# Performance work log

Hardware: AMD Instinct MI355X
Metric: run time of the kernel (lower is better)

## Reference

```python
import jax, jax.numpy as jnp
import numpy as np

SPARSITY = 0.8
LOCAL_WINDOW = 64


def setup_inputs() -> dict:
    key = jax.random.key(0)
    k1, k2 = jax.random.split(key)
    B, H, S = 2, 8, 2048
    attention_scores = jax.random.normal(k1, (B, H, S, S), dtype=jnp.float32)
    rand_u = jax.random.uniform(k2, (B, H, S, S), dtype=jnp.float32)
    return {"attention_scores": attention_scores, "rand_u": rand_u}


def reference(attention_scores, rand_u):
    B, H, S, _ = attention_scores.shape
    dt = attention_scores.dtype
    half = LOCAL_WINDOW // 2
    k = max(1, int(S * (1.0 - SPARSITY)))

    idx = jnp.arange(S)
    # local window mask: row i covers columns [max(0,i-half), min(S,i+half))
    local = ((idx[None, :] >= idx[:, None] - half) & (idx[None, :] < idx[:, None] + half)).astype(dt)  # (S,S)

    # global mask: topk over head-averaged importance, shared across heads
    importance = attention_scores.mean(axis=1)  # (B,S,S)
    _, top_g = jax.lax.top_k(importance, k)  # (B,S,k)
    gmask = jnp.zeros((B, S, S), dtype=dt).at[
        jnp.arange(B)[:, None, None], jnp.arange(S)[None, :, None], top_g
    ].set(1.0)

    # random sparsification mask
    random_mask = (rand_u < (1.0 - SPARSITY)).astype(dt)

    combined = ((local[None, None, :, :] + gmask[:, None, :, :] + random_mask) > 0).astype(dt)

    # sparsity enforcement: per-row topk of masked scores -> binary mask
    masked = attention_scores * combined
    _, top_f = jax.lax.top_k(masked, k)  # (B,H,S,k)
    final = jnp.zeros((B, H, S, S), dtype=dt).at[
        jnp.arange(B)[:, None, None, None],
        jnp.arange(H)[None, :, None, None],
        jnp.arange(S)[None, None, :, None],
        top_f,
    ].set(1.0)
    return final
```

## Files before the change

kernel.cpp:

```cpp
#include <hip/hip_runtime.h>
#include <cstdint>
#include <cstddef>

#define S_LEN   2048
#define N_HEADS 8
#define N_BATCH 2
#define TOPK    409
#define HALF_WIN 32
#define KEY_P0  0x80000000u
#define KEY_N0  0x7FFFFFFFu

__device__ __forceinline__ unsigned mbcnt64(unsigned long long m) {
  return __builtin_amdgcn_mbcnt_hi((unsigned)(m >> 32),
         __builtin_amdgcn_mbcnt_lo((unsigned)m, 0u));
}

__device__ __forceinline__ void radix_range(const unsigned (&keys)[32], unsigned kk0,
                                            bool pos, unsigned* h, int l,
                                            unsigned& T_ret, unsigned& kk_ret,
                                            bool& cnt1) {
  unsigned prefix = 0, done = 0, kk = kk0;
  unsigned T = 0;
  bool resolved = false;
  cnt1 = false;
  #pragma unroll
  for (int pass = 0; pass < 4; ++pass) {
    const int shift = 24 - 8 * pass;
    *(uint4*)&h[l * 4] = make_uint4(0, 0, 0, 0);
    __threadfence_block();
    #pragma unroll
    for (int q = 0; q < 32; ++q) {
      unsigned kj = keys[q];
      bool in = pos ? (kj > KEY_P0) : (kj < KEY_N0);
      if (in && (kj & done) == prefix)
        atomicAdd(&h[(kj >> shift) & 255u], 1u);
    }
    __threadfence_block();
    uint4 hv = *(const uint4*)&h[l * 4];
    unsigned s3 = hv.w;
    unsigned s2 = hv.z + s3;
    unsigned s1 = hv.y + s2;
    unsigned s0 = hv.x + s1;
    unsigned inc = s0;
    #pragma unroll
    for (int d = 1; d < 64; d <<= 1) {
      unsigned o = __shfl_down(inc, d);
      inc += (l + d < 64) ? o : 0u;
    }
    const unsigned tail = inc - s0;
    const unsigned ge[4] = {s0 + tail, s1 + tail, s2 + tail, s3 + tail};
    const unsigned gt[4] = {s1 + tail, s2 + tail, s3 + tail, tail};
    unsigned packed = 0;
    bool found = false;
    #pragma unroll
    for (int q = 0; q < 4; ++q) {
      if (gt[q] < kk && kk <= ge[q]) {
        packed = ((unsigned)(4 * l + q) << 24) | ((ge[q] - gt[q]) << 12) | (kk - gt[q]);
        found = true;
      }
    }
    unsigned long long bal = __ballot(found);
    int srcl = __ffsll((long long)bal) - 1;
    packed = __shfl(packed, srcl);
    const unsigned cnt = (packed >> 12) & 0xFFFu;
    kk = packed & 0xFFFu;
    prefix |= (packed >> 24) << shift;
    done |= 0xFFu << shift;
    if (cnt == 1u) {
      unsigned cand = 0;
      #pragma unroll
      for (int q = 0; q < 32; ++q) {
        unsigned kj = keys[q];
        bool in = pos ? (kj > KEY_P0) : (kj < KEY_N0);
        if (in && (kj & done) == prefix) cand = kj;
      }
      #pragma unroll
      for (int d = 1; d < 64; d <<= 1) cand |= __shfl_xor(cand, d);
      T = cand;
      resolved = true;
      cnt1 = true;
      break;
    }
  }
  if (!resolved) T = prefix;
  T_ret = T;
  kk_ret = kk;
}

__device__ __forceinline__ void resolve_T(const unsigned (&keys)[32], unsigned* h,
                                          int l, unsigned& T, unsigned& kk,
                                          bool& cnt1) {
  unsigned np = 0;
  #pragma unroll
  for (int q = 0; q < 32; ++q)
    np += (unsigned)__popcll(__ballot(keys[q] > KEY_P0));
  if (TOPK <= np) {
    radix_range(keys, TOPK, true, h, l, T, kk, cnt1);
  } else {
    unsigned n0 = 0, n1 = 0;
    #pragma unroll
    for (int q = 0; q < 32; ++q) {
      n0 += (unsigned)__popcll(__ballot(keys[q] == KEY_P0));
      n1 += (unsigned)__popcll(__ballot(keys[q] == KEY_N0));
    }
    if (TOPK <= np + n0)           { T = KEY_P0; kk = TOPK - np;      cnt1 = (n0 == 1); }
    else if (TOPK <= np + n0 + n1) { T = KEY_N0; kk = TOPK - np - n0; cnt1 = (n1 == 1); }
    else radix_range(keys, TOPK - np - n0 - n1, false, h, l, T, kk, cnt1);
  }
}

__device__ __forceinline__ unsigned select_bits(const unsigned (&keys)[32],
                                                unsigned T, unsigned kk,
                                                bool cnt1, int l) {
  unsigned bits = 0;
  if (cnt1) {
    #pragma unroll
    for (int q = 0; q < 32; ++q)
      bits |= (keys[q] >= T ? 1u : 0u) << q;
    return bits;
  }
  unsigned S_tot = 0;
  #pragma unroll
  for (int s = 0; s < 8; ++s) {
    unsigned long long beq[4];
    unsigned pe[4];
    #pragma unroll
    for (int e = 0; e < 4; ++e) {
      beq[e] = __ballot(keys[4 * s + e] == T);
      pe[e] = (unsigned)__popcll(beq[e]);
    }
    const unsigned th = pe[0] + pe[1] + pe[2] + pe[3];
    if (S_tot + th <= kk) {
      #pragma unroll
      for (int e = 0; e < 4; ++e)
        bits |= (keys[4 * s + e] >= T ? 1u : 0u) << (4 * s + e);
    } else if (S_tot >= kk) {
      #pragma unroll
      for (int e = 0; e < 4; ++e)
        bits |= (keys[4 * s + e] > T ? 1u : 0u) << (4 * s + e);
    } else {
      unsigned mb[4], own[4];
      #pragma unroll
      for (int e = 0; e < 4; ++e) {
        mb[e]  = mbcnt64(beq[e]);
        own[e] = (unsigned)((beq[e] >> l) & 1ull);
      }
      const unsigned cross = S_tot + mb[0] + mb[1] + mb[2] + mb[3];
      unsigned run = 0;
      #pragma unroll
      for (int e = 0; e < 4; ++e) {
        unsigned kj = keys[4 * s + e];
        bool sel = (kj > T) || (kj == T && (cross + run) < kk);
        run += own[e];
        bits |= (sel ? 1u : 0u) << (4 * s + e);
      }
    }
    S_tot += th;
  }
  return bits;
}

__global__ __launch_bounds__(512, 4) void k_fused(const float* __restrict__ scores,
                                                  const float* __restrict__ randu,
                                                  float* __restrict__ out) {
  __shared__ __align__(16) float sc_lds[N_HEADS][S_LEN];
  __shared__ __align__(16) unsigned hist[N_HEADS][256];
  __shared__ unsigned char gbytes[512];
  const int l = threadIdx.x & 63;
  const int w = threadIdx.x >> 6;
  const int bi = blockIdx.x;
  const int b = bi >> 11;
  const int i = bi & 2047;
  const size_t row = (((size_t)(b * N_HEADS + w)) * S_LEN + i) * S_LEN;
  const float thr = (float)(1.0 - 0.8);

  unsigned rndbits = 0;
  #pragma unroll
  for (int s = 0; s < 8; ++s) {
    const int j0 = 256 * s + 4 * l;
    float4 sc = *(const float4*)(scores + row + j0);
    float4 ru = *(const float4*)(randu + row + j0);
    *(float4*)&sc_lds[w][j0] = sc;
    rndbits |= (ru.x < thr ? 1u : 0u) << (4 * s + 0);
    rndbits |= (ru.y < thr ? 1u : 0u) << (4 * s + 1);
    rndbits |= (ru.z < thr ? 1u : 0u) << (4 * s + 2);
    rndbits |= (ru.w < thr ? 1u : 0u) << (4 * s + 3);
  }
  __syncthreads();

  if (w == 0) {
    unsigned gkeys[32];
    #pragma unroll
    for (int s = 0; s < 8; ++s) {
      const int j0 = 256 * s + 4 * l;
      float4 a = *(const float4*)&sc_lds[0][j0];
      #pragma unroll
      for (int hh = 1; hh < N_HEADS; ++hh) {
        float4 x = *(const float4*)&sc_lds[hh][j0];
        a.x += x.x; a.y += x.y; a.z += x.z; a.w += x.w;
      }
      const float av[4] = {a.x, a.y, a.z, a.w};
      #pragma unroll
      for (int e = 0; e < 4; ++e) {
        unsigned u = __float_as_uint(av[e]);
        gkeys[4 * s + e] = (u & 0x80000000u) ? ~u : (u | 0x80000000u);
      }
    }
    unsigned T, kk; bool cnt1;
    resolve_T(gkeys, hist[0], l, T, kk, cnt1);
    unsigned bits = select_bits(gkeys, T, kk, cnt1, l);
    const int lo = i - HALF_WIN;
    #pragma unroll
    for (int s = 0; s < 8; ++s) {
      const int j0 = 256 * s + 4 * l;
      unsigned nib = (bits >> (4 * s)) & 0xFu;
      #pragma unroll
      for (int e = 0; e < 4; ++e)
        nib |= ((unsigned)(j0 + e - lo) < 64u ? 1u : 0u) << e;
      gbytes[64 * s + l] = (unsigned char)nib;
    }
  }
  __syncthreads();

  unsigned keys[32];
  #pragma unroll
  for (int s = 0; s < 8; ++s) {
    const int j0 = 256 * s + 4 * l;
    float4 sc = *(const float4*)&sc_lds[w][j0];
    const unsigned cn = (unsigned)gbytes[64 * s + l] | ((rndbits >> (4 * s)) & 0xFu);
    const float scv[4] = {sc.x, sc.y, sc.z, sc.w};
    #pragma unroll
    for (int e = 0; e < 4; ++e) {
      const unsigned u = __float_as_uint(scv[e]);
      const unsigned m = (unsigned)((int)u >> 31) | 0x80000000u;
      const bool comb = ((cn >> e) & 1u) != 0u;
      keys[4 * s + e] = (comb ? u : (u & 0x80000000u)) ^ m;
    }
  }
  unsigned T, kk; bool cnt1;
  resolve_T(keys, hist[w], l, T, kk, cnt1);
  unsigned bits = select_bits(keys, T, kk, cnt1, l);
  #pragma unroll
  for (int s = 0; s < 8; ++s) {
    float v[4] __attribute__((aligned(16)));
    #pragma unroll
    for (int e = 0; e < 4; ++e)
      v[e] = ((bits >> (4 * s + e)) & 1u) ? 1.0f : 0.0f;
    *(float4*)(out + row + 256 * s + 4 * l) = *(const float4*)v;
  }
}

extern "C" void kernel_launch(void* const* d_in, const int* in_sizes, int n_in,
                              void* d_out, int out_size, void* d_ws, size_t ws_size,
                              hipStream_t stream) {
  const float* scores = (const float*)d_in[0];
  const float* randu  = (const float*)d_in[1];
  float* out = (float*)d_out;
  (void)d_ws; (void)ws_size;
  k_fused<<<N_BATCH * S_LEN, 512, 0, stream>>>(scores, randu, out);
}
```

Baseline: 210.2 us.

## Parallelize global top-k across all waves and shrink LDS staging to raise occupancy

Removes the serial phase in which only wave 0 computed the head-summed importance and its top-k while seven waves idled. All eight waves now split the head sum by column slice and each redundantly runs the global top-k from a shared LDS key array. Score rows stay in registers, and only a four-row staging buffer is used, written in two rounds, which cuts LDS per block so launch bounds can rise to 6. The cost is extra barriers, redundant selection work, and more register pressure from holding 32 keys per lane.

```diff
diff --git a/kernel.cpp b/kernel.cpp
--- a/kernel.cpp
+++ b/kernel.cpp
@@ -15,10 +15,16 @@
          __builtin_amdgcn_mbcnt_lo((unsigned)m, 0u));
 }
 
-__device__ __forceinline__ void radix_range(const unsigned (&keys)[32], unsigned kk0,
-                                            bool pos, unsigned* h, int l,
-                                            unsigned& T_ret, unsigned& kk_ret,
-                                            bool& cnt1) {
+__device__ __forceinline__ unsigned mono1(float f) {
+  unsigned u = __float_as_uint(f);
+  return (u & 0x80000000u) ? ~u : (u | 0x80000000u);
+}
+
+template <class G>
+__device__ __forceinline__ void radix_rangeT(G get, unsigned kk0, bool pos,
+                                             unsigned* h, int l,
+                                             unsigned& T_ret, unsigned& kk_ret,
+                                             bool& cnt1) {
   unsigned prefix = 0, done = 0, kk = kk0;
   unsigned T = 0;
   bool resolved = false;
@@ -30,7 +36,7 @@
     __threadfence_block();
     #pragma unroll
     for (int q = 0; q < 32; ++q) {
-      unsigned kj = keys[q];
+      unsigned kj = get(q);
       bool in = pos ? (kj > KEY_P0) : (kj < KEY_N0);
       if (in && (kj & done) == prefix)
         atomicAdd(&h[(kj >> shift) & 255u], 1u);
@@ -70,7 +76,7 @@
       unsigned cand = 0;
       #pragma unroll
       for (int q = 0; q < 32; ++q) {
-        unsigned kj = keys[q];
+        unsigned kj = get(q);
         bool in = pos ? (kj > KEY_P0) : (kj < KEY_N0);
         if (in && (kj & done) == prefix) cand = kj;
       }
@@ -87,36 +93,37 @@
   kk_ret = kk;
 }
 
-__device__ __forceinline__ void resolve_T(const unsigned (&keys)[32], unsigned* h,
-                                          int l, unsigned& T, unsigned& kk,
-                                          bool& cnt1) {
+template <class G>
+__device__ __forceinline__ void resolve_TT(G get, unsigned* h, int l,
+                                           unsigned& T, unsigned& kk, bool& cnt1) {
   unsigned np = 0;
   #pragma unroll
   for (int q = 0; q < 32; ++q)
-    np += (unsigned)__popcll(__ballot(keys[q] > KEY_P0));
+    np += (unsigned)__popcll(__ballot(get(q) > KEY_P0));
   if (TOPK <= np) {
-    radix_range(keys, TOPK, true, h, l, T, kk, cnt1);
+    radix_rangeT(get, TOPK, true, h, l, T, kk, cnt1);
   } else {
     unsigned n0 = 0, n1 = 0;
     #pragma unroll
     for (int q = 0; q < 32; ++q) {
-      n0 += (unsigned)__popcll(__ballot(keys[q] == KEY_P0));
-      n1 += (unsigned)__popcll(__ballot(keys[q] == KEY_N0));
+      unsigned kj = get(q);
+      n0 += (unsigned)__popcll(__ballot(kj == KEY_P0));
+      n1 += (unsigned)__popcll(__ballot(kj == KEY_N0));
     }
     if (TOPK <= np + n0)           { T = KEY_P0; kk = TOPK - np;      cnt1 = (n0 == 1); }
     else if (TOPK <= np + n0 + n1) { T = KEY_N0; kk = TOPK - np - n0; cnt1 = (n1 == 1); }
-    else radix_range(keys, TOPK - np - n0 - n1, false, h, l, T, kk, cnt1);
-  }
-}
-
-__device__ __forceinline__ unsigned select_bits(const unsigned (&keys)[32],
-                                                unsigned T, unsigned kk,
-                                                bool cnt1, int l) {
+    else radix_rangeT(get, TOPK - np - n0 - n1, false, h, l, T, kk, cnt1);
+  }
+}
+
+template <class G>
+__device__ __forceinline__ unsigned select_bitsT(G get, unsigned T, unsigned kk,
+                                                 bool cnt1, int l) {
   unsigned bits = 0;
   if (cnt1) {
     #pragma unroll
     for (int q = 0; q < 32; ++q)
-      bits |= (keys[q] >= T ? 1u : 0u) << q;
+      bits |= (get(q) >= T ? 1u : 0u) << q;
     return bits;
   }
   unsigned S_tot = 0;
@@ -126,18 +133,18 @@
     unsigned pe[4];
     #pragma unroll
     for (int e = 0; e < 4; ++e) {
-      beq[e] = __ballot(keys[4 * s + e] == T);
+      beq[e] = __ballot(get(4 * s + e) == T);
       pe[e] = (unsigned)__popcll(beq[e]);
     }
     const unsigned th = pe[0] + pe[1] + pe[2] + pe[3];
     if (S_tot + th <= kk) {
       #pragma unroll
       for (int e = 0; e < 4; ++e)
-        bits |= (keys[4 * s + e] >= T ? 1u : 0u) << (4 * s + e);
+        bits |= (get(4 * s + e) >= T ? 1u : 0u) << (4 * s + e);
     } else if (S_tot >= kk) {
       #pragma unroll
       for (int e = 0; e < 4; ++e)
-        bits |= (keys[4 * s + e] > T ? 1u : 0u) << (4 * s + e);
+        bits |= (get(4 * s + e) > T ? 1u : 0u) << (4 * s + e);
     } else {
       unsigned mb[4], own[4];
       #pragma unroll
@@ -149,7 +156,7 @@
       unsigned run = 0;
       #pragma unroll
       for (int e = 0; e < 4; ++e) {
-        unsigned kj = keys[4 * s + e];
+        unsigned kj = get(4 * s + e);
         bool sel = (kj > T) || (kj == T && (cross + run) < kk);
         run += own[e];
         bits |= (sel ? 1u : 0u) << (4 * s + e);
@@ -160,12 +167,12 @@
   return bits;
 }
 
-__global__ __launch_bounds__(512, 4) void k_fused(const float* __restrict__ scores,
+__global__ __launch_bounds__(512, 6) void k_fused(const float* __restrict__ scores,
                                                   const float* __restrict__ randu,
                                                   float* __restrict__ out) {
-  __shared__ __align__(16) float sc_lds[N_HEADS][S_LEN];
+  __shared__ __align__(16) float stage[4][S_LEN];
+  __shared__ __align__(16) unsigned gsum[S_LEN];
   __shared__ __align__(16) unsigned hist[N_HEADS][256];
-  __shared__ unsigned char gbytes[512];
   const int l = threadIdx.x & 63;
   const int w = threadIdx.x >> 6;
   const int bi = blockIdx.x;
@@ -174,72 +181,85 @@
   const size_t row = (((size_t)(b * N_HEADS + w)) * S_LEN + i) * S_LEN;
   const float thr = (float)(1.0 - 0.8);
 
+  unsigned sb[32];
   unsigned rndbits = 0;
   #pragma unroll
   for (int s = 0; s < 8; ++s) {
     const int j0 = 256 * s + 4 * l;
     float4 sc = *(const float4*)(scores + row + j0);
     float4 ru = *(const float4*)(randu + row + j0);
-    *(float4*)&sc_lds[w][j0] = sc;
+    sb[4 * s + 0] = __float_as_uint(sc.x);
+    sb[4 * s + 1] = __float_as_uint(sc.y);
+    sb[4 * s + 2] = __float_as_uint(sc.z);
+    sb[4 * s + 3] = __float_as_uint(sc.w);
     rndbits |= (ru.x < thr ? 1u : 0u) << (4 * s + 0);
     rndbits |= (ru.y < thr ? 1u : 0u) << (4 * s + 1);
     rndbits |= (ru.z < thr ? 1u : 0u) << (4 * s + 2);
     rndbits |= (ru.w < thr ? 1u : 0u) << (4 * s + 3);
-  }
-  __syncthreads();
-
-  if (w == 0) {
-    unsigned gkeys[32];
-    #pragma unroll
-    for (int s = 0; s < 8; ++s) {
-      const int j0 = 256 * s + 4 * l;
-      float4 a = *(const float4*)&sc_lds[0][j0];
-      #pragma unroll
-      for (int hh = 1; hh < N_HEADS; ++hh) {
-        float4 x = *(const float4*)&sc_lds[hh][j0];
-        a.x += x.x; a.y += x.y; a.z += x.z; a.w += x.w;
-      }
-      const float av[4] = {a.x, a.y, a.z, a.w};
-      #pragma unroll
-      for (int e = 0; e < 4; ++e) {
-        unsigned u = __float_as_uint(av[e]);
-        gkeys[4 * s + e] = (u & 0x80000000u) ? ~u : (u | 0x80000000u);
-      }
-    }
-    unsigned T, kk; bool cnt1;
-    resolve_T(gkeys, hist[0], l, T, kk, cnt1);
-    unsigned bits = select_bits(gkeys, T, kk, cnt1, l);
+    if (w < 4) *(float4*)&stage[w][j0] = sc;
+  }
+  __syncthreads();
+
+  {
+    const int c0 = 256 * w + 4 * l;
+    float4 a = *(const float4*)&stage[0][c0];
+    #pragma unroll
+    for (int hh = 1; hh < 4; ++hh) {
+      float4 x = *(const float4*)&stage[hh][c0];
+      a.x += x.x; a.y += x.y; a.z += x.z; a.w += x.w;
+    }
+    *(float4*)&gsum[c0] = a;
+  }
+  __syncthreads();
+
+  if (w >= 4) {
+    #pragma unroll
+    for (int s = 0; s < 8; ++s)
+      *(uint4*)&stage[w - 4][256 * s + 4 * l] = *(const uint4*)&sb[4 * s];
+  }
+  __syncthreads();
+
+  {
+    const int c0 = 256 * w + 4 * l;
+    float4 a = *(const float4*)&gsum[c0];
+    #pragma unroll
+    for (int hh = 0; hh < 4; ++hh) {
+      float4 x = *(const float4*)&stage[hh][c0];
+      a.x += x.x; a.y += x.y; a.z += x.z; a.w += x.w;
+    }
+    uint4 kq;
+    kq.x = mono1(a.x); kq.y = mono1(a.y); kq.z = mono1(a.z); kq.w = mono1(a.w);
+    *(uint4*)&gsum[c0] = kq;
+  }
+  __syncthreads();
+
+  auto getG = [&](int q) -> unsigned {
+    return gsum[256 * (q >> 2) + 4 * l + (q & 3)];
+  };
+  unsigned Tg, kkg; bool c1g;
+  resolve_TT(getG, hist[w], l, Tg, kkg, c1g);
+  unsigned gbits = select_bitsT(getG, Tg, kkg, c1g, l);
+  {
     const int lo = i - HALF_WIN;
     #pragma unroll
-    for (int s = 0; s < 8; ++s) {
-      const int j0 = 256 * s + 4 * l;
-      unsigned nib = (bits >> (4 * s)) & 0xFu;
-      #pragma unroll
-      for (int e = 0; e < 4; ++e)
-        nib |= ((unsigned)(j0 + e - lo) < 64u ? 1u : 0u) << e;
-      gbytes[64 * s + l] = (unsigned char)nib;
-    }
-  }
-  __syncthreads();
-
-  unsigned keys[32];
-  #pragma unroll
-  for (int s = 0; s < 8; ++s) {
-    const int j0 = 256 * s + 4 * l;
-    float4 sc = *(const float4*)&sc_lds[w][j0];
-    const unsigned cn = (unsigned)gbytes[64 * s + l] | ((rndbits >> (4 * s)) & 0xFu);
-    const float scv[4] = {sc.x, sc.y, sc.z, sc.w};
-    #pragma unroll
-    for (int e = 0; e < 4; ++e) {
-      const unsigned u = __float_as_uint(scv[e]);
-      const unsigned m = (unsigned)((int)u >> 31) | 0x80000000u;
-      const bool comb = ((cn >> e) & 1u) != 0u;
-      keys[4 * s + e] = (comb ? u : (u & 0x80000000u)) ^ m;
-    }
-  }
-  unsigned T, kk; bool cnt1;
-  resolve_T(keys, hist[w], l, T, kk, cnt1);
-  unsigned bits = select_bits(keys, T, kk, cnt1, l);
+    for (int q = 0; q < 32; ++q) {
+      const int j = 256 * (q >> 2) + 4 * l + (q & 3);
+      gbits |= ((unsigned)(j - lo) < 64u ? 1u : 0u) << q;
+    }
+  }
+  const unsigned combined = gbits | rndbits;
+
+  #pragma unroll
+  for (int q = 0; q < 32; ++q) {
+    const unsigned u = sb[q];
+    const unsigned m = (unsigned)((int)u >> 31) | 0x80000000u;
+    const bool comb = ((combined >> q) & 1u) != 0u;
+    sb[q] = (comb ? u : (u & 0x80000000u)) ^ m;
+  }
+  auto getK = [&](int q) -> unsigned { return sb[q]; };
+  unsigned T, kk; bool c1;
+  resolve_TT(getK, hist[w], l, T, kk, c1);
+  unsigned bits = select_bitsT(getK, T, kk, c1, l);
   #pragma unroll
   for (int s = 0; s < 8; ++s) {
     float v[4] __attribute__((aligned(16)));
```

New measurement: 282.3 us. 34.3% more time.
